# Performance work log

Hardware: AMD Instinct MI355X
Metric: run time of the kernel (lower is better)

The kernel has to match this reference:

```python
import jax, jax.numpy as jnp
import numpy as np

B, S, E, H = 2, 2048, 1024, 16
D = E // H  # head_dim = 64


def setup_inputs() -> dict:
    key = jax.random.key(0)
    ks = jax.random.split(key, 6)
    sc = 0.02
    return {
        "hidden_states": jax.random.normal(ks[0], (B, S, E), dtype=jnp.float32),
        "attn_bias": jax.random.normal(ks[1], (S, S), dtype=jnp.float32) * sc,
        "Wqkv": jax.random.normal(ks[2], (E, 3 * E), dtype=jnp.float32) * sc,
        "bqkv": jax.random.normal(ks[3], (3 * E,), dtype=jnp.float32) * sc,
        "Wproj": jax.random.normal(ks[4], (E, E), dtype=jnp.float32) * sc,
        "bproj": jax.random.normal(ks[5], (E,), dtype=jnp.float32) * sc,
    }


def reference(hidden_states, attn_bias, Wqkv, bqkv, Wproj, bproj):
    b, s, e = hidden_states.shape
    qkv = hidden_states @ Wqkv + bqkv                      # [b,s,3e]
    q, k, v = jnp.split(qkv, 3, axis=-1)                   # each [b,s,e]
    cache_key, cache_value = k, v                          # kvCache
    # [b,h,s,d]
    qh = q.reshape(b, s, H, D).transpose(0, 2, 1, 3)
    kh = k.reshape(b, s, H, D).transpose(0, 2, 1, 3)
    vh = v.reshape(b, s, H, D).transpose(0, 2, 1, 3)
    scores = jnp.einsum("bhqd,bhkd->bhqk", qh, kh) / jnp.sqrt(jnp.float32(D))
    scores = scores + attn_bias[:s, :s][None, None]        # learned additive bias
    causal = jnp.tril(jnp.ones((s, s), dtype=bool))
    scores = jnp.where(causal[None, None], scores, jnp.float32(-1e9))
    attn = jax.nn.softmax(scores, axis=-1)
    ctx = jnp.einsum("bhqk,bhkd->bhqd", attn, vh)
    ctx = ctx.transpose(0, 2, 1, 3).reshape(b, s, e)
    out = ctx @ Wproj + bproj                              # resid dropout p=0 -> identity
    return (out, cache_key, cache_value)
```

## Files before the change

kernel.cpp:

```cpp
#include <hip/hip_runtime.h>

#define B_ 2
#define S_ 2048
#define E_ 1024
#define H_ 16
#define D_ 64

typedef short  s16x8 __attribute__((ext_vector_type(8)));
typedef float  f32x4 __attribute__((ext_vector_type(4)));
typedef unsigned short u16x4 __attribute__((ext_vector_type(4)));

__device__ __forceinline__ ushort f2bf(float f) {
    union { float f; unsigned u; } x; x.f = f;
    unsigned u = x.u + 0x7fffu + ((x.u >> 16) & 1u);
    return (ushort)(u >> 16);
}

__device__ __forceinline__ float fast_exp2(float x) {
    float r; asm("v_exp_f32 %0, %1" : "=v"(r) : "v"(x)); return r;
}

__global__ __launch_bounds__(256) void prep_fused_kernel(
    const float* __restrict__ X, ushort* __restrict__ Xbf,
    const float* __restrict__ Wqkv, ushort* __restrict__ Wqkvt,
    const float* __restrict__ Wproj, ushort* __restrict__ Wprojt)
{
    __shared__ float tile[64][65];
    int blk = blockIdx.x;
    int tid = threadIdx.x;
    if (blk < 4096) {
        int i = (blk * 256 + tid) * 4;
        float4 v = *(const float4*)&X[i];
        u16x4 o;
        o.x = f2bf(v.x); o.y = f2bf(v.y); o.z = f2bf(v.z); o.w = f2bf(v.w);
        *(u16x4*)&Xbf[i] = o;
        return;
    }
    const float* W; ushort* Wt; int Ndim, nb;
    if (blk < 4096 + 768) { blk -= 4096; W = Wqkv;  Wt = Wqkvt;  Ndim = 3 * E_; nb = 48; }
    else                  { blk -= 4864; W = Wproj; Wt = Wprojt; Ndim = E_;     nb = 16; }
    int n0 = (blk % nb) * 64, k0 = (blk / nb) * 64;
    int c = tid & 63;
#pragma unroll
    for (int r = tid >> 6; r < 64; r += 4)
        tile[r][c] = W[(size_t)(k0 + r) * Ndim + n0 + c];
    __syncthreads();
#pragma unroll
    for (int r = tid >> 6; r < 64; r += 4)
        Wt[(size_t)(n0 + r) * E_ + k0 + c] = f2bf(tile[c][r]);
}

__global__ __launch_bounds__(256) void post_qkv_kernel(
    const float* __restrict__ V, ushort* __restrict__ Vt,
    const float* __restrict__ bias, ushort* __restrict__ biasT)
{
    __shared__ float tile[64][65];
    int blk = blockIdx.x;
    int tid = threadIdx.x;
    if (blk < 1024) {
        int s0 = (blk & 31) * 64;
        int bh = blk >> 5;
        int b = bh >> 4, h = bh & 15;
        int d = tid & 63;
#pragma unroll
        for (int i = tid >> 6; i < 64; i += 4)
            tile[i][d] = V[((size_t)(b * S_ + s0 + i)) * E_ + h * 64 + d];
        __syncthreads();
        int lane = tid & 63, w = tid >> 6;
        int src = ((lane & 3) * 16) + (lane >> 2);
#pragma unroll
        for (int dd = w; dd < 64; dd += 4)
            Vt[((size_t)(bh * 64 + dd)) * S_ + s0 + lane] = f2bf(tile[src][dd]);
        return;
    }
    int L = blk - 1024;
    int qi = (int)((sqrtf(8.0f * (float)L + 1.0f) - 1.0f) * 0.5f);
    while ((qi + 1) * (qi + 2) / 2 <= L) qi++;
    while (qi * (qi + 1) / 2 > L) qi--;
    int ki = L - qi * (qi + 1) / 2;
    int w = tid >> 6, quad = (tid >> 4) & 3, l15 = tid & 15;
    const float LOG2E = 1.4426950408889634f;
    s16x8 h0 = (s16x8){0,0,0,0,0,0,0,0}, h1 = (s16x8){0,0,0,0,0,0,0,0};
#pragma unroll
    for (int r = 0; r < 4; r++)
#pragma unroll
        for (int kt = 0; kt < 4; kt++) {
            float v = bias[(size_t)(qi * 64 + w * 16 + quad * 4 + r) * S_
                           + ki * 64 + kt * 16 + l15] * LOG2E;
            ushort u = f2bf(v);
            int idx = r * 4 + kt;
            if (idx < 8) h0[idx] = (short)u; else h1[idx - 8] = (short)u;
        }
    ushort* dst = &biasT[((size_t)L * 256 + tid) * 16];
    *(s16x8*)dst = h0;
    *(s16x8*)(dst + 8) = h1;
}

__global__ __launch_bounds__(256) void gemm_mfma_bt(
    const ushort* __restrict__ A,
    const ushort* __restrict__ Bt,
    const float* __restrict__ bias,
    int M, int N, int K,
    float* __restrict__ C0,
    ushort* __restrict__ Qbf, float* __restrict__ Kf32, ushort* __restrict__ Kbf,
    float* __restrict__ Vf32, int mode)
{
    __shared__ ushort As[128 * 64];
    __shared__ ushort Bs[128 * 64];
    int tid = threadIdx.x;
    int wid = tid >> 6, lane = tid & 63;
    int l15 = lane & 15, quad = lane >> 4;
    int wm = wid >> 1, wn = wid & 1;
    int row0 = blockIdx.y * 128, col0 = blockIdx.x * 128;

    int srow = tid >> 3;
    int pk = (tid & 7) * 8;
    int sk = (((tid & 7) ^ (srow & 7)) * 8);

    f32x4 acc[4][4];
#pragma unroll
    for (int mt = 0; mt < 4; mt++)
#pragma unroll
        for (int nt = 0; nt < 4; nt++) acc[mt][nt] = (f32x4){0.f, 0.f, 0.f, 0.f};

    for (int k0 = 0; k0 < K; k0 += 64) {
        __syncthreads();
#pragma unroll
        for (int c = 0; c < 4; c++) {
            int r = c * 32 + srow;
            __builtin_amdgcn_global_load_lds(
                (const __attribute__((address_space(1))) unsigned int*)
                    &A[(size_t)(row0 + r) * K + k0 + sk],
                (__attribute__((address_space(3))) unsigned int*)&As[r * 64 + pk],
                16, 0, 0);
            __builtin_amdgcn_global_load_lds(
                (const __attribute__((address_space(1))) unsigned int*)
                    &Bt[(size_t)(col0 + r) * K + k0 + sk],
                (__attribute__((address_space(3))) unsigned int*)&Bs[r * 64 + pk],
                16, 0, 0);
        }
        __syncthreads();

#pragma unroll
        for (int kk = 0; kk < 2; kk++) {
            int xc = (((kk * 4 + quad) ^ (l15 & 7)) * 8);
            s16x8 af[4], bf[4];
#pragma unroll
            for (int mt = 0; mt < 4; mt++)
                af[mt] = *(const s16x8*)&As[(wm * 64 + mt * 16 + l15) * 64 + xc];
#pragma unroll
            for (int nt = 0; nt < 4; nt++)
                bf[nt] = *(const s16x8*)&Bs[(wn * 64 + nt * 16 + l15) * 64 + xc];
#pragma unroll
            for (int mt = 0; mt < 4; mt++)
#pragma unroll
                for (int nt = 0; nt < 4; nt++)
                    acc[mt][nt] = __builtin_amdgcn_mfma_f32_16x16x32_bf16(
                        af[mt], bf[nt], acc[mt][nt], 0, 0, 0);
        }
    }

#pragma unroll
    for (int nt = 0; nt < 4; nt++) {
        int n = col0 + wn * 64 + nt * 16 + l15;
        float bv = bias[n];
        if (mode == 1) {
            int seg = n >> 10;
            int nn = n & (E_ - 1);
#pragma unroll
            for (int mt = 0; mt < 4; mt++)
#pragma unroll
                for (int r = 0; r < 4; r++) {
                    int row = row0 + wm * 64 + mt * 16 + quad * 4 + r;
                    float v = acc[mt][nt][r] + bv;
                    size_t idx = (size_t)row * E_ + nn;
                    if (seg == 0)      Qbf[idx] = f2bf(v);
                    else if (seg == 1) { Kf32[idx] = v; Kbf[idx] = f2bf(v); }
                    else               Vf32[idx] = v;
                }
        } else {
#pragma unroll
            for (int mt = 0; mt < 4; mt++)
#pragma unroll
                for (int r = 0; r < 4; r++) {
                    int row = row0 + wm * 64 + mt * 16 + quad * 4 + r;
                    C0[(size_t)row * N + n] = acc[mt][nt][r] + bv;
                }
        }
    }
}

__global__ __launch_bounds__(256) void attn_mfma_kernel(
    const ushort* __restrict__ Qbf,
    const ushort* __restrict__ Kbf,
    const ushort* __restrict__ Vt,
    const ushort* __restrict__ biasT,
    ushort* __restrict__ Ctx)
{
    __shared__ ushort Ks[2][64][64];
    __shared__ ushort Vs[2][64][64];
    __shared__ ushort Ps[4][16][72];

    int blk = blockIdx.x;
    int bh = blk & 31;
    int pr = blk >> 5;
    int b = bh >> 4, h = bh & 15;
    int tid = threadIdx.x;
    int wid = tid >> 6, lane = tid & 63;
    int l15 = lane & 15, quad = lane >> 4;

    int skey = tid >> 2;
    int scol = (tid & 3) * 16;
    int sc0 = ((((tid & 3) * 2) ^ (skey & 7)) * 8);
    int sc1 = sc0 ^ 8;
    const float scale_l2e = 0.18033688011112042f;

    const size_t krow = (size_t)(b * S_ + skey) * E_ + h * 64 + scol;
    const size_t vrow = (size_t)(bh * 64 + skey) * S_ + scol;
    int rc0 = (quad ^ (l15 & 7)) * 8;

    for (int half = 0; half < 2; half++) {
        int qt = half ? pr : (31 - pr);
        int q0w = qt * 64 + wid * 16;

        const size_t qbase = ((size_t)(b * S_ + q0w + l15)) * E_ + h * 64 + quad * 8;
        s16x8 qa0 = *(const s16x8*)&Qbf[qbase];
        s16x8 qa1 = *(const s16x8*)&Qbf[qbase + 32];

        f32x4 o[4];
#pragma unroll
        for (int dt = 0; dt < 4; dt++) o[dt] = (f32x4){0.f, 0.f, 0.f, 0.f};
        float lsum[4];
#pragma unroll
        for (int r = 0; r < 4; r++) lsum[r] = 0.f;

        {
            float4 k0a = ((const float4*)&Kbf[krow])[0];
            float4 k0b = ((const float4*)&Kbf[krow])[1];
            float4 v0a = ((const float4*)&Vt[vrow])[0];
            float4 v0b = ((const float4*)&Vt[vrow])[1];
            *(float4*)&Ks[0][skey][sc0] = k0a;
            *(float4*)&Ks[0][skey][sc1] = k0b;
            *(float4*)&Vs[0][skey][sc0] = v0a;
            *(float4*)&Vs[0][skey][sc1] = v0b;
        }
        float4 kr0, kr1, vr0, vr1;
        if (qt >= 1) {
            kr0 = ((const float4*)&Kbf[krow + (size_t)64 * E_])[0];
            kr1 = ((const float4*)&Kbf[krow + (size_t)64 * E_])[1];
            vr0 = ((const float4*)&Vt[vrow + 64])[0];
            vr1 = ((const float4*)&Vt[vrow + 64])[1];
        }
        const ushort* bt = &biasT[((size_t)(qt * (qt + 1) / 2) * 256 + tid) * 16];
        s16x8 bn0 = *(const s16x8*)bt;
        s16x8 bn1 = *(const s16x8*)(bt + 8);
        __syncthreads();

        for (int t = 0; t <= qt; t++) {
            int j0 = t * 64;
            int cur = t & 1, nxt = cur ^ 1;

            if (t < qt) {
                *(float4*)&Ks[nxt][skey][sc0] = kr0;
                *(float4*)&Ks[nxt][skey][sc1] = kr1;
                *(float4*)&Vs[nxt][skey][sc0] = vr0;
                *(float4*)&Vs[nxt][skey][sc1] = vr1;
            }
            if (t + 2 <= qt) {
                size_t koff = krow + (size_t)((t + 2) * 64) * E_;
                kr0 = ((const float4*)&Kbf[koff])[0];
                kr1 = ((const float4*)&Kbf[koff])[1];
                vr0 = ((const float4*)&Vt[vrow + (t + 2) * 64])[0];
                vr1 = ((const float4*)&Vt[vrow + (t + 2) * 64])[1];
            }
            s16x8 b0 = bn0, b1 = bn1;
            if (t < qt) {
                const ushort* btn = bt + (size_t)(t + 1) * 4096;
                bn0 = *(const s16x8*)btn;
                bn1 = *(const s16x8*)(btn + 8);
            }

            f32x4 s[4];
#pragma unroll
            for (int kt = 0; kt < 4; kt++) {
                s16x8 kb0 = *(const s16x8*)&Ks[cur][kt * 16 + l15][rc0];
                s16x8 kb1 = *(const s16x8*)&Ks[cur][kt * 16 + l15][rc0 ^ 32];
                f32x4 acc = (f32x4){0.f, 0.f, 0.f, 0.f};
                acc = __builtin_amdgcn_mfma_f32_16x16x32_bf16(qa0, kb0, acc, 0, 0, 0);
                acc = __builtin_amdgcn_mfma_f32_16x16x32_bf16(qa1, kb1, acc, 0, 0, 0);
                s[kt] = acc;
            }

            bool diag = (t == qt);
#pragma unroll
            for (int r = 0; r < 4; r++) {
                int row = q0w + quad * 4 + r;
                float pv[4];
#pragma unroll
                for (int kt = 0; kt < 4; kt++) {
                    int j = j0 + kt * 16 + l15;
                    int idx = r * 4 + kt;
                    ushort ub = (ushort)((idx < 8) ? b0[idx] : b1[idx - 8]);
                    union { unsigned u; float f; } bc; bc.u = ((unsigned)ub) << 16;
                    float v = fmaf(s[kt][r], scale_l2e, bc.f);
                    float p = (diag && j > row) ? 0.f : fast_exp2(v);
                    lsum[r] += p;
                    pv[kt] = p;
                }
                unsigned w0, w1;
                asm("v_cvt_pk_bf16_f32 %0, %1, %2" : "=v"(w0) : "v"(pv[0]), "v"(pv[1]));
                asm("v_cvt_pk_bf16_f32 %0, %1, %2" : "=v"(w1) : "v"(pv[2]), "v"(pv[3]));
                uint2 wv; wv.x = w0; wv.y = w1;
                *(uint2*)&Ps[wid][quad * 4 + r][l15 * 4] = wv;
            }

            s16x8 pa0 = *(const s16x8*)&Ps[wid][l15][quad * 8];
            s16x8 pa1 = *(const s16x8*)&Ps[wid][l15][32 + quad * 8];
#pragma unroll
            for (int dt = 0; dt < 4; dt++) {
                s16x8 vb0 = *(const s16x8*)&Vs[cur][dt * 16 + l15][rc0];
                s16x8 vb1 = *(const s16x8*)&Vs[cur][dt * 16 + l15][rc0 ^ 32];
                o[dt] = __builtin_amdgcn_mfma_f32_16x16x32_bf16(pa0, vb0, o[dt], 0, 0, 0);
                o[dt] = __builtin_amdgcn_mfma_f32_16x16x32_bf16(pa1, vb1, o[dt], 0, 0, 0);
            }

            __syncthreads();
        }

        float inv_l[4];
#pragma unroll
        for (int r = 0; r < 4; r++) {
            float l = lsum[r];
            l += __shfl_xor(l, 1);
            l += __shfl_xor(l, 2);
            l += __shfl_xor(l, 4);
            l += __shfl_xor(l, 8);
            inv_l[r] = 1.f / l;
        }

#pragma unroll
        for (int dt = 0; dt < 4; dt++) {
#pragma unroll
            for (int r = 0; r < 4; r++) {
                int row = q0w + quad * 4 + r;
                Ctx[((size_t)(b * S_ + row)) * E_ + h * 64 + dt * 16 + l15] =
                    f2bf(o[dt][r] * inv_l[r]);
            }
        }
    }
}

extern "C" void kernel_launch(void* const* d_in, const int* in_sizes, int n_in,
                              void* d_out, int out_size, void* d_ws, size_t ws_size,
                              hipStream_t stream) {
    const float* X     = (const float*)d_in[0];
    const float* abias = (const float*)d_in[1];
    const float* Wqkv  = (const float*)d_in[2];
    const float* bqkv  = (const float*)d_in[3];
    const float* Wproj = (const float*)d_in[4];
    const float* bproj = (const float*)d_in[5];

    const size_t plane = (size_t)B_ * S_ * E_;
    float* out  = (float*)d_out;
    float* kout = out + plane;
    float* vout = kout + plane;

    ushort* xbf    = (ushort*)d_ws;
    ushort* qbf    = xbf + plane;
    ushort* kbf    = qbf + plane;
    ushort* vt     = kbf + plane;
    ushort* ctxbf  = xbf;
    ushort* wqkvt  = vt + plane;
    ushort* wprojt = wqkvt + (size_t)3 * E_ * E_;
    ushort* biasT  = wqkvt;

    const int M = B_ * S_;

    prep_fused_kernel<<<dim3(5120), 256, 0, stream>>>(
        X, xbf, Wqkv, wqkvt, Wproj, wprojt);

    gemm_mfma_bt<<<dim3(3 * E_ / 128, M / 128), 256, 0, stream>>>(
        xbf, wqkvt, bqkv, M, 3 * E_, E_,
        nullptr, qbf, kout, kbf, vout, 1);

    post_qkv_kernel<<<dim3(1024 + 528), 256, 0, stream>>>(
        vout, vt, abias, biasT);

    attn_mfma_kernel<<<dim3(B_ * H_ * 16), 256, 0, stream>>>(
        qbf, kbf, vt, biasT, ctxbf);

    gemm_mfma_bt<<<dim3(E_ / 128, M / 128), 256, 0, stream>>>(
        ctxbf, wprojt, bproj, M, E_, E_,
        out, nullptr, nullptr, nullptr, nullptr, 0);
}
```

Measured before the change: 211.8 us.

## Process two KV tiles per barrier pair with register-prefetched pair loads

```diff
diff --git a/kernel.cpp b/kernel.cpp
--- a/kernel.cpp
+++ b/kernel.cpp
@@ -197,8 +197,8 @@
     const ushort* __restrict__ biasT,
     ushort* __restrict__ Ctx)
 {
-    __shared__ ushort Ks[2][64][64];
-    __shared__ ushort Vs[2][64][64];
+    __shared__ ushort Ks[128][64];
+    __shared__ ushort Vs[128][64];
     __shared__ ushort Ps[4][16][72];
 
     int blk = blockIdx.x;
@@ -222,6 +222,7 @@
     for (int half = 0; half < 2; half++) {
         int qt = half ? pr : (31 - pr);
         int q0w = qt * 64 + wid * 16;
+        int U = (qt + 2) >> 1;
 
         const size_t qbase = ((size_t)(b * S_ + q0w + l15)) * E_ + h * 64 + quad * 8;
         s16x8 qa0 = *(const s16x8*)&Qbf[qbase];
@@ -234,97 +235,109 @@
 #pragma unroll
         for (int r = 0; r < 4; r++) lsum[r] = 0.f;
 
-        {
-            float4 k0a = ((const float4*)&Kbf[krow])[0];
-            float4 k0b = ((const float4*)&Kbf[krow])[1];
-            float4 v0a = ((const float4*)&Vt[vrow])[0];
-            float4 v0b = ((const float4*)&Vt[vrow])[1];
-            *(float4*)&Ks[0][skey][sc0] = k0a;
-            *(float4*)&Ks[0][skey][sc1] = k0b;
-            *(float4*)&Vs[0][skey][sc0] = v0a;
-            *(float4*)&Vs[0][skey][sc1] = v0b;
-        }
-        float4 kr0, kr1, vr0, vr1;
-        if (qt >= 1) {
-            kr0 = ((const float4*)&Kbf[krow + (size_t)64 * E_])[0];
-            kr1 = ((const float4*)&Kbf[krow + (size_t)64 * E_])[1];
-            vr0 = ((const float4*)&Vt[vrow + 64])[0];
-            vr1 = ((const float4*)&Vt[vrow + 64])[1];
-        }
+        int t1p = (qt >= 1) ? 1 : 0;
+        float4 k0a = ((const float4*)&Kbf[krow])[0];
+        float4 k0b = ((const float4*)&Kbf[krow])[1];
+        float4 v0a = ((const float4*)&Vt[vrow])[0];
+        float4 v0b = ((const float4*)&Vt[vrow])[1];
+        float4 k1a = ((const float4*)&Kbf[krow + (size_t)(t1p * 64) * E_])[0];
+        float4 k1b = ((const float4*)&Kbf[krow + (size_t)(t1p * 64) * E_])[1];
+        float4 v1a = ((const float4*)&Vt[vrow + t1p * 64])[0];
+        float4 v1b = ((const float4*)&Vt[vrow + t1p * 64])[1];
         const ushort* bt = &biasT[((size_t)(qt * (qt + 1) / 2) * 256 + tid) * 16];
-        s16x8 bn0 = *(const s16x8*)bt;
-        s16x8 bn1 = *(const s16x8*)(bt + 8);
-        __syncthreads();
-
-        for (int t = 0; t <= qt; t++) {
-            int j0 = t * 64;
-            int cur = t & 1, nxt = cur ^ 1;
-
-            if (t < qt) {
-                *(float4*)&Ks[nxt][skey][sc0] = kr0;
-                *(float4*)&Ks[nxt][skey][sc1] = kr1;
-                *(float4*)&Vs[nxt][skey][sc0] = vr0;
-                *(float4*)&Vs[nxt][skey][sc1] = vr1;
+        s16x8 bn00 = *(const s16x8*)bt;
+        s16x8 bn01 = *(const s16x8*)(bt + 8);
+        const ushort* btp = bt + (size_t)t1p * 4096;
+        s16x8 bn10 = *(const s16x8*)btp;
+        s16x8 bn11 = *(const s16x8*)(btp + 8);
+
+        for (int u = 0; u < U; u++) {
+            int tb = 2 * u;
+            __syncthreads();
+            *(float4*)&Ks[skey][sc0]      = k0a;
+            *(float4*)&Ks[skey][sc1]      = k0b;
+            *(float4*)&Vs[skey][sc0]      = v0a;
+            *(float4*)&Vs[skey][sc1]      = v0b;
+            *(float4*)&Ks[64 + skey][sc0] = k1a;
+            *(float4*)&Ks[64 + skey][sc1] = k1b;
+            *(float4*)&Vs[64 + skey][sc0] = v1a;
+            *(float4*)&Vs[64 + skey][sc1] = v1b;
+            s16x8 bc[2][2];
+            bc[0][0] = bn00; bc[0][1] = bn01;
+            bc[1][0] = bn10; bc[1][1] = bn11;
+            __syncthreads();
+
+            if (u + 1 < U) {
+                int ta = 2 * u + 2;
+                int tbn = (2 * u + 3 <= qt) ? (2 * u + 3) : qt;
+                size_t ka = krow + (size_t)(ta * 64) * E_;
+                size_t kb_ = krow + (size_t)(tbn * 64) * E_;
+                k0a = ((const float4*)&Kbf[ka])[0];
+                k0b = ((const float4*)&Kbf[ka])[1];
+                v0a = ((const float4*)&Vt[vrow + ta * 64])[0];
+                v0b = ((const float4*)&Vt[vrow + ta * 64])[1];
+                k1a = ((const float4*)&Kbf[kb_])[0];
+                k1b = ((const float4*)&Kbf[kb_])[1];
+                v1a = ((const float4*)&Vt[vrow + tbn * 64])[0];
+                v1b = ((const float4*)&Vt[vrow + tbn * 64])[1];
+                const ushort* pa = bt + (size_t)ta * 4096;
+                bn00 = *(const s16x8*)pa;
+                bn01 = *(const s16x8*)(pa + 8);
+                const ushort* pb = bt + (size_t)tbn * 4096;
+                bn10 = *(const s16x8*)pb;
+                bn11 = *(const s16x8*)(pb + 8);
             }
-            if (t + 2 <= qt) {
-                size_t koff = krow + (size_t)((t + 2) * 64) * E_;
-                kr0 = ((const float4*)&Kbf[koff])[0];
-                kr1 = ((const float4*)&Kbf[koff])[1];
-                vr0 = ((const float4*)&Vt[vrow + (t + 2) * 64])[0];
-                vr1 = ((const float4*)&Vt[vrow + (t + 2) * 64])[1];
+
+#pragma unroll
+            for (int sub = 0; sub < 2; sub++) {
+                int t = tb + sub;
+                if (t > qt) continue;
+                int j0 = t * 64;
+                bool diag = (t == qt);
+
+                f32x4 s[4];
+#pragma unroll
+                for (int kt = 0; kt < 4; kt++) {
+                    s16x8 kb0 = *(const s16x8*)&Ks[sub * 64 + kt * 16 + l15][rc0];
+                    s16x8 kb1 = *(const s16x8*)&Ks[sub * 64 + kt * 16 + l15][rc0 ^ 32];
+                    f32x4 acc = (f32x4){0.f, 0.f, 0.f, 0.f};
+                    acc = __builtin_amdgcn_mfma_f32_16x16x32_bf16(qa0, kb0, acc, 0, 0, 0);
+                    acc = __builtin_amdgcn_mfma_f32_16x16x32_bf16(qa1, kb1, acc, 0, 0, 0);
+                    s[kt] = acc;
+                }
+
+#pragma unroll
+                for (int r = 0; r < 4; r++) {
+                    int row = q0w + quad * 4 + r;
+                    float pv[4];
+#pragma unroll
+                    for (int kt = 0; kt < 4; kt++) {
+                        int j = j0 + kt * 16 + l15;
+                        int idx = r * 4 + kt;
+                        ushort ub = (ushort)((idx < 8) ? bc[sub][0][idx] : bc[sub][1][idx - 8]);
+                        union { unsigned u; float f; } bcv; bcv.u = ((unsigned)ub) << 16;
+                        float v = fmaf(s[kt][r], scale_l2e, bcv.f);
+                        float p = (diag && j > row) ? 0.f : fast_exp2(v);
+                        lsum[r] += p;
+                        pv[kt] = p;
+                    }
+                    unsigned w0, w1;
+                    asm("v_cvt_pk_bf16_f32 %0, %1, %2" : "=v"(w0) : "v"(pv[0]), "v"(pv[1]));
+                    asm("v_cvt_pk_bf16_f32 %0, %1, %2" : "=v"(w1) : "v"(pv[2]), "v"(pv[3]));
+                    uint2 wv; wv.x = w0; wv.y = w1;
+                    *(uint2*)&Ps[wid][quad * 4 + r][l15 * 4] = wv;
+                }
+
+                s16x8 pa0 = *(const s16x8*)&Ps[wid][l15][quad * 8];
+                s16x8 pa1 = *(const s16x8*)&Ps[wid][l15][32 + quad * 8];
+#pragma unroll
+                for (int dt = 0; dt < 4; dt++) {
+                    s16x8 vb0 = *(const s16x8*)&Vs[sub * 64 + dt * 16 + l15][rc0];
+                    s16x8 vb1 = *(const s16x8*)&Vs[sub * 64 + dt * 16 + l15][rc0 ^ 32];
+                    o[dt] = __builtin_amdgcn_mfma_f32_16x16x32_bf16(pa0, vb0, o[dt], 0, 0, 0);
+                    o[dt] = __builtin_amdgcn_mfma_f32_16x16x32_bf16(pa1, vb1, o[dt], 0, 0, 0);
+                }
             }
-            s16x8 b0 = bn0, b1 = bn1;
-            if (t < qt) {
-                const ushort* btn = bt + (size_t)(t + 1) * 4096;
-                bn0 = *(const s16x8*)btn;
-                bn1 = *(const s16x8*)(btn + 8);
-            }
-
-            f32x4 s[4];
-#pragma unroll
-            for (int kt = 0; kt < 4; kt++) {
-                s16x8 kb0 = *(const s16x8*)&Ks[cur][kt * 16 + l15][rc0];
-                s16x8 kb1 = *(const s16x8*)&Ks[cur][kt * 16 + l15][rc0 ^ 32];
-                f32x4 acc = (f32x4){0.f, 0.f, 0.f, 0.f};
-                acc = __builtin_amdgcn_mfma_f32_16x16x32_bf16(qa0, kb0, acc, 0, 0, 0);
-                acc = __builtin_amdgcn_mfma_f32_16x16x32_bf16(qa1, kb1, acc, 0, 0, 0);
-                s[kt] = acc;
-            }
-
-            bool diag = (t == qt);
-#pragma unroll
-            for (int r = 0; r < 4; r++) {
-                int row = q0w + quad * 4 + r;
-                float pv[4];
-#pragma unroll
-                for (int kt = 0; kt < 4; kt++) {
-                    int j = j0 + kt * 16 + l15;
-                    int idx = r * 4 + kt;
-                    ushort ub = (ushort)((idx < 8) ? b0[idx] : b1[idx - 8]);
-                    union { unsigned u; float f; } bc; bc.u = ((unsigned)ub) << 16;
-                    float v = fmaf(s[kt][r], scale_l2e, bc.f);
-                    float p = (diag && j > row) ? 0.f : fast_exp2(v);
-                    lsum[r] += p;
-                    pv[kt] = p;
-                }
-                unsigned w0, w1;
-                asm("v_cvt_pk_bf16_f32 %0, %1, %2" : "=v"(w0) : "v"(pv[0]), "v"(pv[1]));
-                asm("v_cvt_pk_bf16_f32 %0, %1, %2" : "=v"(w1) : "v"(pv[2]), "v"(pv[3]));
-                uint2 wv; wv.x = w0; wv.y = w1;
-                *(uint2*)&Ps[wid][quad * 4 + r][l15 * 4] = wv;
-            }
-
-            s16x8 pa0 = *(const s16x8*)&Ps[wid][l15][quad * 8];
-            s16x8 pa1 = *(const s16x8*)&Ps[wid][l15][32 + quad * 8];
-#pragma unroll
-            for (int dt = 0; dt < 4; dt++) {
-                s16x8 vb0 = *(const s16x8*)&Vs[cur][dt * 16 + l15][rc0];
-                s16x8 vb1 = *(const s16x8*)&Vs[cur][dt * 16 + l15][rc0 ^ 32];
-                o[dt] = __builtin_amdgcn_mfma_f32_16x16x32_bf16(pa0, vb0, o[dt], 0, 0, 0);
-                o[dt] = __builtin_amdgcn_mfma_f32_16x16x32_bf16(pa1, vb1, o[dt], 0, 0, 0);
-            }
-
-            __syncthreads();
         }
 
         float inv_l[4];
```

Result: slower. 222.7 us (+5.2%).
